# Performance work log

Measured on AMD Instinct MI355X. Metric: run time of the kernel, lower is better.

## Reference

```python
import jax, jax.numpy as jnp
import numpy as np
import math


def gen_slopes(n_heads, alibi_bias_max=1.0):
    # matches torch gen_slopes: _n_heads = next pow2, m = arange(1.._n)*max/_n, slopes = 2^-m
    _n = 2 ** math.ceil(math.log2(n_heads))
    m = jnp.arange(1, _n + 1, dtype=jnp.float32) * (alibi_bias_max / _n)
    slopes = 1.0 / jnp.power(2.0, m)
    if _n != n_heads:
        slopes = jnp.concatenate([slopes[1::2], slopes[::2]])[:n_heads]
    return slopes.reshape(1, n_heads, 1, 1)


def build_alibi_bias(n_heads, seq_len, alibi_bias_max=1.0):
    # full=False branch: bias over key positions only, shape [1, H, 1, L]
    pos = jnp.arange(1 - seq_len, 1, dtype=jnp.float32).reshape(1, 1, 1, seq_len)
    return pos * gen_slopes(n_heads, alibi_bias_max)


def setup_inputs() -> dict:
    key = jax.random.key(0)
    kq, kk, kv = jax.random.split(key, 3)
    B, L, H, E = 8, 1024, 8, 64
    return {
        "queries": jax.random.normal(kq, (B, L, H, E), dtype=jnp.float32),
        "keys": jax.random.normal(kk, (B, L, H, E), dtype=jnp.float32),
        "values": jax.random.normal(kv, (B, L, H, E), dtype=jnp.float32),
        "patch_index": -1,
    }


def reference(queries, keys, values, patch_index):
    B, L, H, E = queries.shape
    scale = 1.0 / math.sqrt(E)
    # scores: [B, H, L, L]
    scores = jnp.einsum('blhe,bshe->bhls', queries, keys)
    attn = scale * scores + build_alibi_bias(H, L)  # ALiBi bias, alibi_bias_max=1
    series = jax.nn.softmax(attn, axis=-1)  # dropout is identity in eval mode
    V = jnp.einsum('bhls,bshd->blhd', series, values)
    # patch_index == -1: identity branch, series unchanged
    return (V, series)
```

## Files before the change

kernel.cpp:

```cpp
#include <hip/hip_runtime.h>
#include <hip/hip_bf16.h>


typedef short short8 __attribute__((ext_vector_type(8)));
typedef short short4v __attribute__((ext_vector_type(4)));
typedef float f32x4 __attribute__((ext_vector_type(4)));
typedef unsigned short u16x4 __attribute__((ext_vector_type(4)));

#define B_ 8
#define L_ 1024
#define H_ 8
#define E_ 64
#define RSTRIDE (H_ * E_)
#define QBLK 64
#define CHUNK 64
#define NCH (L_ / CHUNK)
#define CHUNK_USH (CHUNK * E_)

__device__ __forceinline__ unsigned short f2bf(float f) {
  return __builtin_bit_cast(unsigned short, __float2bfloat16(f));
}
__device__ __forceinline__ short8 ldfrag(const float* p) {
  float4 a = *reinterpret_cast<const float4*>(p);
  float4 b = *reinterpret_cast<const float4*>(p + 4);
  return (short8){(short)f2bf(a.x), (short)f2bf(a.y), (short)f2bf(a.z),
                  (short)f2bf(a.w), (short)f2bf(b.x), (short)f2bf(b.y),
                  (short)f2bf(b.z), (short)f2bf(b.w)};
}

__device__ __forceinline__ f32x4 mfma16(short4v a, short4v b, f32x4 c) {
#if __has_builtin(__builtin_amdgcn_mfma_f32_16x16x16bf16_1k)
  return __builtin_amdgcn_mfma_f32_16x16x16bf16_1k(a, b, c, 0, 0, 0);
#else
  asm volatile(
      "s_nop 1\n\t"
      "v_mfma_f32_16x16x16_bf16 %0, %1, %2, %0\n\t"
      "s_nop 2"
      : "+v"(c)
      : "v"(a), "v"(b));
  return c;
#endif
}

__device__ __forceinline__ void gld16(const unsigned short* g,
                                      unsigned short* l) {
  __builtin_amdgcn_global_load_lds(
      (const __attribute__((address_space(1))) unsigned int*)g,
      (__attribute__((address_space(3))) unsigned int*)l, 16, 0, 0);
}

__global__ __launch_bounds__(256, 4) void prep_kv(
    const float* __restrict__ Kg, const float* __restrict__ Vg,
    unsigned short* __restrict__ Kbf, unsigned short* __restrict__ VTbf) {
  __shared__ unsigned short vt[64 * 64];

  const int t = threadIdx.x;
  const int id = blockIdx.x;
  const int bh = id & 63;
  const int sc = id >> 6;
  const int h = bh & 7, b = bh >> 3;
  const int s0 = sc * CHUNK;

  const float* Kb = Kg + ((size_t)b * L_ + s0) * RSTRIDE + h * E_;
  const float* Vb = Vg + ((size_t)b * L_ + s0) * RSTRIDE + h * E_;
  unsigned short* Ko = Kbf + (size_t)(bh * NCH + sc) * CHUNK_USH;
  unsigned short* Vo = VTbf + (size_t)(bh * NCH + sc) * CHUNK_USH;

#pragma unroll
  for (int i = 0; i < 2; ++i) {
    const int j = t + 256 * i;
    const int s = j >> 3;
    const int e8 = (j & 7) ^ (s & 7);
    const float* kp = Kb + (size_t)s * RSTRIDE + 8 * e8;
    float4 a = *reinterpret_cast<const float4*>(kp);
    float4 c = *reinterpret_cast<const float4*>(kp + 4);
    *reinterpret_cast<u16x4*>(&Ko[j * 8]) =
        (u16x4){f2bf(a.x), f2bf(a.y), f2bf(a.z), f2bf(a.w)};
    *reinterpret_cast<u16x4*>(&Ko[j * 8 + 4]) =
        (u16x4){f2bf(c.x), f2bf(c.y), f2bf(c.z), f2bf(c.w)};
  }
  {
    const int e = t & 63, w = t >> 6;
#pragma unroll
    for (int i = 0; i < 4; ++i) {
      const int s4 = 4 * w + 16 * i;
      const float* vp = Vb + (size_t)s4 * RSTRIDE + e;
      u16x4 u = {f2bf(vp[0]), f2bf(vp[RSTRIDE]), f2bf(vp[2 * RSTRIDE]),
                 f2bf(vp[3 * RSTRIDE])};
      *reinterpret_cast<u16x4*>(
          &vt[e * 64 + (((s4 >> 3) ^ (e & 7)) << 3) + (s4 & 7)]) = u;
    }
  }
  __syncthreads();
#pragma unroll
  for (int i = 0; i < 2; ++i) {
    const int j = t + 256 * i;
    u16x4 u0 = *reinterpret_cast<const u16x4*>(&vt[j * 8]);
    u16x4 u1 = *reinterpret_cast<const u16x4*>(&vt[j * 8 + 4]);
    *reinterpret_cast<u16x4*>(&Vo[j * 8]) = u0;
    *reinterpret_cast<u16x4*>(&Vo[j * 8 + 4]) = u1;
  }
}

__global__ __launch_bounds__(256, 4) void alibi_attn(
    const float* __restrict__ Qg, const unsigned short* __restrict__ Kbf,
    const unsigned short* __restrict__ VTbf, float* __restrict__ Vout,
    float* __restrict__ Pout) {
  __shared__ unsigned short sK[2][CHUNK_USH];
  __shared__ unsigned short sVT[2][CHUNK_USH];

  const int t = threadIdx.x;
  const int lane = t & 63;
  const int w = t >> 6;
  const int col = lane & 15;
  const int kg = lane >> 4;

  const int id = blockIdx.x;
  const int qb = id >> 6;
  const int bh = id & 63;
  const int h = bh & 7;
  const int b = bh >> 3;
  const int q0 = qb * QBLK;

  const float sc_l2e = 0.125f * 1.44269504f;
  const float sl_l2e = exp2f(-(float)(h + 1) * 0.125f) * 1.44269504f;

  const unsigned short* Kc = Kbf + (size_t)bh * NCH * CHUNK_USH;
  const unsigned short* Vc = VTbf + (size_t)bh * NCH * CHUNK_USH;

  short8 qf0, qf1;
  {
    const float* qp =
        Qg + ((size_t)b * L_ + q0 + 16 * w + col) * RSTRIDE + h * E_ + 8 * kg;
    qf0 = ldfrag(qp);
    qf1 = ldfrag(qp + 32);
  }

  const float kbias0 = sl_l2e * (float)(4 * kg - 1023) - 32.0f;

#define STAGE_K(c, bi)                                                  \
  {                                                                     \
    const unsigned short* src = Kc + (size_t)(c) * CHUNK_USH;           \
    _Pragma("unroll") for (int i = 0; i < 2; ++i) {                     \
      const int seg = i * 4 + w;                                        \
      gld16(src + (size_t)(seg * 64 + lane) * 8, &sK[bi][seg * 512]);   \
    }                                                                   \
  }
#define STAGE_V(c, bi)                                                  \
  {                                                                     \
    const unsigned short* src = Vc + (size_t)(c) * CHUNK_USH;           \
    _Pragma("unroll") for (int i = 0; i < 2; ++i) {                     \
      const int seg = i * 4 + w;                                        \
      gld16(src + (size_t)(seg * 64 + lane) * 8, &sVT[bi][seg * 512]);  \
    }                                                                   \
  }

  float z0 = 0.f, z1 = 0.f, z2 = 0.f, z3 = 0.f;
  STAGE_K(0, 0);
  __syncthreads();
  for (int c = 0; c < NCH; ++c) {
    if (c + 1 < NCH) STAGE_K(c + 1, (c + 1) & 1);
    const unsigned short* kb = sK[c & 1];
#pragma unroll
    for (int kt = 0; kt < 4; ++kt) {
      const int row = 16 * kt + col;
      short8 k0 = *reinterpret_cast<const short8*>(
          &kb[row * 64 + ((kg ^ (row & 7)) << 3)]);
      short8 k1 = *reinterpret_cast<const short8*>(
          &kb[row * 64 + (((kg + 4) ^ (row & 7)) << 3)]);
      f32x4 acc = {0.f, 0.f, 0.f, 0.f};
      acc = __builtin_amdgcn_mfma_f32_16x16x32_bf16(k0, qf0, acc, 0, 0, 0);
      acc = __builtin_amdgcn_mfma_f32_16x16x32_bf16(k1, qf1, acc, 0, 0, 0);
      const float base = fmaf((float)(CHUNK * c + 16 * kt), sl_l2e, kbias0);
      z0 += __builtin_amdgcn_exp2f(fmaf(acc[0], sc_l2e, base));
      z1 += __builtin_amdgcn_exp2f(fmaf(acc[1], sc_l2e, base + sl_l2e));
      z2 += __builtin_amdgcn_exp2f(fmaf(acc[2], sc_l2e, base + 2.f * sl_l2e));
      z3 += __builtin_amdgcn_exp2f(fmaf(acc[3], sc_l2e, base + 3.f * sl_l2e));
    }
    __syncthreads();
  }
  float z = (z0 + z1) + (z2 + z3);
  z += __shfl_xor(z, 16, 64);
  z += __shfl_xor(z, 32, 64);
  const float minv = 1.0f / z;

  f32x4 oacc[4];
#pragma unroll
  for (int et = 0; et < 4; ++et) oacc[et] = (f32x4){0.f, 0.f, 0.f, 0.f};

  float* Pb =
      Pout + ((size_t)(b * H_ + h) * L_ + q0 + 16 * w + col) * L_ + 4 * kg;

  STAGE_K(0, 0);
  STAGE_V(0, 0);
  __syncthreads();
  for (int c = 0; c < NCH; ++c) {
    if (c + 1 < NCH) {
      STAGE_K(c + 1, (c + 1) & 1);
      STAGE_V(c + 1, (c + 1) & 1);
    }
    const unsigned short* kb = sK[c & 1];
    const unsigned short* vb = sVT[c & 1];
#pragma unroll
    for (int kt = 0; kt < 4; ++kt) {
      const int row = 16 * kt + col;
      short8 k0 = *reinterpret_cast<const short8*>(
          &kb[row * 64 + ((kg ^ (row & 7)) << 3)]);
      short8 k1 = *reinterpret_cast<const short8*>(
          &kb[row * 64 + (((kg + 4) ^ (row & 7)) << 3)]);
      f32x4 acc = {0.f, 0.f, 0.f, 0.f};
      acc = __builtin_amdgcn_mfma_f32_16x16x32_bf16(k0, qf0, acc, 0, 0, 0);
      acc = __builtin_amdgcn_mfma_f32_16x16x32_bf16(k1, qf1, acc, 0, 0, 0);
      short4v vf[4];
      const int g0 = 2 * kt + (kg >> 1);
      const int so = 4 * (kg & 1);
#pragma unroll
      for (int et = 0; et < 4; ++et) {
        const int e = 16 * et + col;
        vf[et] = *reinterpret_cast<const short4v*>(
            &vb[e * 64 + ((g0 ^ (e & 7)) << 3) + so]);
      }
      const float base = fmaf((float)(CHUNK * c + 16 * kt), sl_l2e, kbias0);
      f32x4 pf;
      pf[0] = __builtin_amdgcn_exp2f(fmaf(acc[0], sc_l2e, base)) * minv;
      pf[1] =
          __builtin_amdgcn_exp2f(fmaf(acc[1], sc_l2e, base + sl_l2e)) * minv;
      pf[2] = __builtin_amdgcn_exp2f(fmaf(acc[2], sc_l2e, base + 2.f * sl_l2e)) *
              minv;
      pf[3] = __builtin_amdgcn_exp2f(fmaf(acc[3], sc_l2e, base + 3.f * sl_l2e)) *
              minv;
      *reinterpret_cast<f32x4*>(Pb + CHUNK * c + 16 * kt) = pf;
      short4v pa = {(short)f2bf(pf[0]), (short)f2bf(pf[1]), (short)f2bf(pf[2]),
                    (short)f2bf(pf[3])};
#pragma unroll
      for (int et = 0; et < 4; ++et) oacc[et] = mfma16(pa, vf[et], oacc[et]);
    }
    __syncthreads();
  }

  float* Vo = Vout + (((size_t)b * L_ + q0 + 16 * w) * H_ + h) * E_;
#pragma unroll
  for (int et = 0; et < 4; ++et) {
#pragma unroll
    for (int r = 0; r < 4; ++r) {
      __builtin_nontemporal_store(oacc[et][r],
                                  &Vo[(4 * kg + r) * RSTRIDE + 16 * et + col]);
    }
  }
}

extern "C" void kernel_launch(void* const* d_in, const int* in_sizes, int n_in,
                              void* d_out, int out_size, void* d_ws,
                              size_t ws_size, hipStream_t stream) {
  const float* Q = (const float*)d_in[0];
  const float* K = (const float*)d_in[1];
  const float* V = (const float*)d_in[2];
  float* out = (float*)d_out;
  float* Vo = out;
  float* Po = out + (size_t)B_ * L_ * H_ * E_;
  unsigned short* Kbf = (unsigned short*)d_ws;
  unsigned short* VTbf = Kbf + (size_t)B_ * H_ * L_ * E_;
  hipLaunchKernelGGL(prep_kv, dim3(NCH * B_ * H_), dim3(256), 0, stream, K, V,
                     Kbf, VTbf);
  hipLaunchKernelGGL(alibi_attn, dim3((L_ / QBLK) * H_ * B_), dim3(256), 0,
                     stream, Q, Kbf, VTbf, Vo, Po);
}
```

Before: 105.5 us.

## Deepen K prefetch and replace full syncs with partial vmcnt barriers

K and V staging now share one four-slot LDS ring. The first (normaliser) pass prefetches K two chunks ahead, and both passes end each iteration with a barrier that waits only until a given number of memory operations remain, instead of a full __syncthreads drain. Scheduling barriers pin the async LDS loads so the compiler cannot reorder them. The aim is to hide global-to-LDS latency behind the MFMA and exp work. The risk is that the counts passed to vmcnt may be wrong once the P-output global stores also count against vmcnt, which could expose races.

```diff
diff --git a/kernel.cpp b/kernel.cpp
--- a/kernel.cpp
+++ b/kernel.cpp
@@ -49,6 +49,13 @@
       (__attribute__((address_space(3))) unsigned int*)l, 16, 0, 0);
 }
 
+#define BAR_VM(N)                                         \
+  {                                                       \
+    asm volatile("s_waitcnt vmcnt(" #N ")" ::: "memory"); \
+    __builtin_amdgcn_s_barrier();                         \
+    __builtin_amdgcn_sched_barrier(0);                    \
+  }
+
 __global__ __launch_bounds__(256, 4) void prep_kv(
     const float* __restrict__ Kg, const float* __restrict__ Vg,
     unsigned short* __restrict__ Kbf, unsigned short* __restrict__ VTbf) {
@@ -106,8 +113,7 @@
     const float* __restrict__ Qg, const unsigned short* __restrict__ Kbf,
     const unsigned short* __restrict__ VTbf, float* __restrict__ Vout,
     float* __restrict__ Pout) {
-  __shared__ unsigned short sK[2][CHUNK_USH];
-  __shared__ unsigned short sVT[2][CHUNK_USH];
+  __shared__ unsigned short sBuf[4][CHUNK_USH];
 
   const int t = threadIdx.x;
   const int lane = t & 63;
@@ -138,29 +144,27 @@
 
   const float kbias0 = sl_l2e * (float)(4 * kg - 1023) - 32.0f;
 
-#define STAGE_K(c, bi)                                                  \
-  {                                                                     \
-    const unsigned short* src = Kc + (size_t)(c) * CHUNK_USH;           \
-    _Pragma("unroll") for (int i = 0; i < 2; ++i) {                     \
-      const int seg = i * 4 + w;                                        \
-      gld16(src + (size_t)(seg * 64 + lane) * 8, &sK[bi][seg * 512]);   \
-    }                                                                   \
-  }
-#define STAGE_V(c, bi)                                                  \
-  {                                                                     \
-    const unsigned short* src = Vc + (size_t)(c) * CHUNK_USH;           \
-    _Pragma("unroll") for (int i = 0; i < 2; ++i) {                     \
-      const int seg = i * 4 + w;                                        \
-      gld16(src + (size_t)(seg * 64 + lane) * 8, &sVT[bi][seg * 512]);  \
-    }                                                                   \
-  }
+#define STAGE(srcbase, c, dst)                                       \
+  {                                                                  \
+    const unsigned short* src = (srcbase) + (size_t)(c)*CHUNK_USH;   \
+    _Pragma("unroll") for (int i = 0; i < 2; ++i) {                  \
+      const int seg = i * 4 + w;                                     \
+      gld16(src + (size_t)(seg * 64 + lane) * 8, (dst) + seg * 512); \
+    }                                                                \
+  }
+#define PIN() __builtin_amdgcn_sched_barrier(0)
 
   float z0 = 0.f, z1 = 0.f, z2 = 0.f, z3 = 0.f;
-  STAGE_K(0, 0);
-  __syncthreads();
+  STAGE(Kc, 0, sBuf[0]);
+  STAGE(Kc, 1, sBuf[1]);
+  PIN();
+  BAR_VM(2);
   for (int c = 0; c < NCH; ++c) {
-    if (c + 1 < NCH) STAGE_K(c + 1, (c + 1) & 1);
-    const unsigned short* kb = sK[c & 1];
+    if (c + 2 < NCH) {
+      STAGE(Kc, c + 2, sBuf[(c + 2) & 3]);
+      PIN();
+    }
+    const unsigned short* kb = sBuf[c & 3];
 #pragma unroll
     for (int kt = 0; kt < 4; ++kt) {
       const int row = 16 * kt + col;
@@ -177,7 +181,11 @@
       z2 += __builtin_amdgcn_exp2f(fmaf(acc[2], sc_l2e, base + 2.f * sl_l2e));
       z3 += __builtin_amdgcn_exp2f(fmaf(acc[3], sc_l2e, base + 3.f * sl_l2e));
     }
-    __syncthreads();
+    if (c + 2 < NCH) {
+      BAR_VM(2);
+    } else {
+      BAR_VM(0);
+    }
   }
   float z = (z0 + z1) + (z2 + z3);
   z += __shfl_xor(z, 16, 64);
@@ -191,16 +199,19 @@
   float* Pb =
       Pout + ((size_t)(b * H_ + h) * L_ + q0 + 16 * w + col) * L_ + 4 * kg;
 
-  STAGE_K(0, 0);
-  STAGE_V(0, 0);
   __syncthreads();
+  STAGE(Kc, 0, sBuf[0]);
+  STAGE(Vc, 0, sBuf[2]);
+  PIN();
+  BAR_VM(0);
   for (int c = 0; c < NCH; ++c) {
     if (c + 1 < NCH) {
-      STAGE_K(c + 1, (c + 1) & 1);
-      STAGE_V(c + 1, (c + 1) & 1);
-    }
-    const unsigned short* kb = sK[c & 1];
-    const unsigned short* vb = sVT[c & 1];
+      STAGE(Kc, c + 1, sBuf[(c + 1) & 1]);
+      STAGE(Vc, c + 1, sBuf[2 + ((c + 1) & 1)]);
+      PIN();
+    }
+    const unsigned short* kb = sBuf[c & 1];
+    const unsigned short* vb = sBuf[2 + (c & 1)];
 #pragma unroll
     for (int kt = 0; kt < 4; ++kt) {
       const int row = 16 * kt + col;
@@ -235,7 +246,7 @@
 #pragma unroll
       for (int et = 0; et < 4; ++et) oacc[et] = mfma16(pa, vf[et], oacc[et]);
     }
-    __syncthreads();
+    BAR_VM(4);
   }
 
   float* Vo = Vout + (((size_t)b * L_ + q0 + 16 * w) * H_ + h) * E_;
```

After: 95.36 us. -9.6%, faster.
